# Kernel tuning notes

Measured on AMD Instinct MI355X. Metric: run time of the kernel, lower is better.

## Reference

```python
import itertools
import jax, jax.numpy as jnp
import numpy as np

# static block configuration
B, C, H, W, DIM, HEADS = 2, 4, 60, 120, 512, 8
WS = (2, 6, 12)          # window size (Wc, Wh, Ww)
SS = (1, 3, 6)           # shift size
N = WS[0] * WS[1] * WS[2]            # 144 tokens per window
C1, H1, W1 = C // WS[0], H // WS[1], W // WS[2]
NW = C1 * H1 * W1                    # windows per sample
DH = DIM // HEADS
EPS = 1e-6


def _attn_bias():
    """Static shifted-window attention bias (nW, N, N): 0 within group, -inf across.
    Mirrors compute_3d_shifted_window_mask (warped=True, longitude wrap merge)."""
    img = np.zeros((C, H, W), np.int32)
    c_sl = ((0, C - WS[0]), (C - WS[0], C - SS[0]), (C - SS[0], C))
    h_sl = ((0, H - WS[1]), (H - WS[1], H - SS[1]), (H - SS[1], H))
    w_sl = ((0, W - WS[2]), (W - WS[2], W - SS[2]), (W - SS[2], W))
    cnt = 0
    for (cs, ce), (hs, he), (ws_, we) in itertools.product(c_sl, h_sl, w_sl):
        img[cs:ce, hs:he, ws_:we] = cnt
        cnt += 1
    # warped (periodic longitude) group merges
    for i in range(3):
        for a, b in ((1, 2), (4, 5), (7, 8)):
            img[img == a + 9 * i] = b + 9 * i
    m = img.reshape(C1, WS[0], H1, WS[1], W1, WS[2])
    m = m.transpose(0, 2, 4, 1, 3, 5).reshape(NW, N)
    diff = m[:, None, :] - m[:, :, None]
    return jnp.asarray(np.where(diff != 0, -np.inf, 0.0).astype(np.float32))


_BIAS = _attn_bias()[None, :, None, :, :]  # (1, nW, 1, N, N)


def _ln(x, s, b):
    mu = x.mean(-1, keepdims=True)
    var = x.var(-1, keepdims=True)
    return (x - mu) / jnp.sqrt(var + EPS) * s + b


def setup_inputs() -> dict:
    key = jax.random.key(0)
    ks = jax.random.split(key, 6)
    s = 0.02
    return {
        "x": jax.random.normal(ks[0], (B, C * H * W, DIM), jnp.float32),
        "qkv_w": jax.random.normal(ks[1], (DIM, 3 * DIM), jnp.float32) * s,
        "qkv_b": jnp.zeros((3 * DIM,), jnp.float32),
        "proj_w": jax.random.normal(ks[2], (DIM, DIM), jnp.float32) * s,
        "proj_b": jnp.zeros((DIM,), jnp.float32),
        "norm1_scale": jnp.ones((DIM,), jnp.float32),
        "norm1_bias": jnp.zeros((DIM,), jnp.float32),
        "norm2_scale": jnp.ones((DIM,), jnp.float32),
        "norm2_bias": jnp.zeros((DIM,), jnp.float32),
        "mlp_w1": jax.random.normal(ks[3], (DIM, 4 * DIM), jnp.float32) * s,
        "mlp_b1": jnp.zeros((4 * DIM,), jnp.float32),
        "mlp_w2": jax.random.normal(ks[4], (4 * DIM, DIM), jnp.float32) * s,
        "mlp_b2": jnp.zeros((DIM,), jnp.float32),
    }


def reference(x, qkv_w, qkv_b, proj_w, proj_b, norm1_scale, norm1_bias,
              norm2_scale, norm2_bias, mlp_w1, mlp_b1, mlp_w2, mlp_b2):
    shortcut = x                                   # (B, L, D)
    h = _ln(x, norm1_scale, norm1_bias).reshape(B, C, H, W, DIM)
    # cyclic shift
    h = jnp.roll(h, (-SS[0], -SS[1], -SS[2]), axis=(1, 2, 3))
    # window partition: (B,C,H,W,D) -> (B*nW, N, D)
    h = h.reshape(B, C1, WS[0], H1, WS[1], W1, WS[2], DIM)
    h = h.transpose(0, 1, 3, 5, 2, 4, 6, 7).reshape(B * NW, N, DIM)
    # windowed multi-head self-attention
    qkv = h @ qkv_w + qkv_b                        # (B*nW, N, 3*D)
    qkv = qkv.reshape(B, NW, N, 3, HEADS, DH)
    q = qkv[..., 0, :, :].transpose(0, 1, 3, 2, 4)  # (B, nW, H, N, Dh)
    k = qkv[..., 1, :, :].transpose(0, 1, 3, 2, 4)
    v = qkv[..., 2, :, :].transpose(0, 1, 3, 2, 4)
    scale = 1.0 / float(np.sqrt(DH))
    attn = jnp.einsum("bwhnd,bwhmd->bwhnm", q, k) * scale + _BIAS
    attn = jax.nn.softmax(attn, axis=-1)
    o = jnp.einsum("bwhnm,bwhmd->bwhnd", attn, v)
    o = o.transpose(0, 1, 3, 2, 4).reshape(B * NW, N, DIM)
    o = o @ proj_w + proj_b
    # window reverse: (B*nW, N, D) -> (B,C,H,W,D)
    o = o.reshape(B, C1, H1, W1, WS[0], WS[1], WS[2], DIM)
    o = o.transpose(0, 1, 4, 2, 5, 3, 6, 7).reshape(B, C, H, W, DIM)
    # reverse cyclic shift
    o = jnp.roll(o, SS, axis=(1, 2, 3))
    x = shortcut + o.reshape(B, C * H * W, DIM)    # drop_path is identity
    # MLP block
    h2 = _ln(x, norm2_scale, norm2_bias)
    h2 = jax.nn.gelu(h2 @ mlp_w1 + mlp_b1) @ mlp_w2 + mlp_b2
    return x + h2
```

## Files before the change

kernel.cpp:

```cpp
#include <hip/hip_runtime.h>

typedef __attribute__((ext_vector_type(8))) short bf16x8;
typedef __attribute__((ext_vector_type(4))) float f32x4;
typedef __attribute__((ext_vector_type(8))) unsigned short u16x8;

#define BAR() __builtin_amdgcn_s_barrier()
#define VMC(n) asm volatile("s_waitcnt vmcnt(" #n ")" ::: "memory")
#define SB0() __builtin_amdgcn_sched_barrier(0)
#define WAITL() do { asm volatile("s_waitcnt lgkmcnt(0)"); SB0(); } while (0)
#define DSRI(dst, base, imm) \
  asm volatile("ds_read_b128 %0, %1 offset:%2" : "=&v"(dst) : "v"(base), "i"(imm))

__device__ inline unsigned short f2bf(float f) {
  unsigned int u = __float_as_uint(f);
  u += 0x7fffu + ((u >> 16) & 1u);
  return (unsigned short)(u >> 16);
}

__device__ inline void gload_lds16(const void* g, void* l) {
  __builtin_amdgcn_global_load_lds(
      (const __attribute__((address_space(1))) void*)g,
      (__attribute__((address_space(3))) void*)l, 16, 0, 0);
}

__global__ void wtrans(const float* __restrict__ W, unsigned short* __restrict__ Wt,
                       int K, int N) {
  int idx = blockIdx.x * 256 + threadIdx.x;
  if (idx >= K * N) return;
  int k = idx / N, n = idx - k * N;
  Wt[(size_t)n * K + k] = f2bf(W[idx]);
}

template <int MODE>
__global__ void ln_k(const float* __restrict__ x, const float* __restrict__ sc,
                     const float* __restrict__ bi, unsigned short* __restrict__ o) {
  int t = blockIdx.x * 4 + (threadIdx.x >> 6);
  int l = threadIdx.x & 63;
  size_t src;
  if (MODE == 0) {
    int b = t / 28800, r = t - b * 28800;
    int win = r / 144, tok = r - win * 144;
    int c1 = win / 100, rem = win - c1 * 100;
    int h1 = rem / 10, w1 = rem - h1 * 10;
    int tc = tok / 72, tr = tok - tc * 72;
    int th = tr / 12, tw = tr - th * 12;
    int cs = c1 * 2 + tc, hs = h1 * 6 + th, wsp = w1 * 12 + tw;
    int co = (cs + 1) & 3;
    int ho = hs + 3; if (ho >= 60) ho -= 60;
    int wo = wsp + 6; if (wo >= 120) wo -= 120;
    src = ((size_t)b * 28800 + (co * 60 + ho) * 120 + wo) * 512;
  } else {
    src = (size_t)t * 512;
  }
  const float4* xr = (const float4*)(x + src);
  float4 v0 = xr[l * 2], v1 = xr[l * 2 + 1];
  float s = v0.x + v0.y + v0.z + v0.w + v1.x + v1.y + v1.z + v1.w;
  float s2 = v0.x * v0.x + v0.y * v0.y + v0.z * v0.z + v0.w * v0.w +
             v1.x * v1.x + v1.y * v1.y + v1.z * v1.z + v1.w * v1.w;
  #pragma unroll
  for (int o2 = 32; o2; o2 >>= 1) {
    s += __shfl_xor(s, o2);
    s2 += __shfl_xor(s2, o2);
  }
  float mean = s * (1.0f / 512.0f);
  float var = s2 * (1.0f / 512.0f) - mean * mean;
  float inv = rsqrtf(var + 1e-6f);
  const float4* scp = (const float4*)sc;
  const float4* bip = (const float4*)bi;
  float4 sa = scp[l * 2], sb = scp[l * 2 + 1];
  float4 ba = bip[l * 2], bb = bip[l * 2 + 1];
  u16x8 ov;
  ov[0] = f2bf((v0.x - mean) * inv * sa.x + ba.x);
  ov[1] = f2bf((v0.y - mean) * inv * sa.y + ba.y);
  ov[2] = f2bf((v0.z - mean) * inv * sa.z + ba.z);
  ov[3] = f2bf((v0.w - mean) * inv * sa.w + ba.w);
  ov[4] = f2bf((v1.x - mean) * inv * sb.x + bb.x);
  ov[5] = f2bf((v1.y - mean) * inv * sb.y + bb.y);
  ov[6] = f2bf((v1.z - mean) * inv * sb.z + bb.z);
  ov[7] = f2bf((v1.w - mean) * inv * sb.w + bb.w);
  *(u16x8*)&o[(size_t)t * 512 + l * 8] = ov;
}

template <int EPI>
__launch_bounds__(256, 2)
__global__ void gemmB(const unsigned short* __restrict__ A,
                      const unsigned short* __restrict__ Bt,
                      const float* __restrict__ bias, void* __restrict__ outp,
                      const float* __restrict__ res, int M, int N, int K) {
  __shared__ __attribute__((aligned(16))) unsigned short ldsA[3][4096];
  const int tid = threadIdx.x;
  const int w = tid >> 6, l = tid & 63;
  const int lane15 = l & 15, lk = (l >> 4) << 3;
  const int ntile = N >> 8;
  const int nwg = gridDim.x;
  const int q = nwg >> 3, r = nwg & 7;
  const int xcd = blockIdx.x & 7, idx8 = blockIdx.x >> 3;
  const int wgid = (xcd < r ? xcd * (q + 1) : r * (q + 1) + (xcd - r) * q) + idx8;
  const int bm = wgid / ntile, bn = wgid - bm * ntile;
  const int KT = K >> 5;

  const int swzb = ((l >> 3) & 3) << 3;
  const int colx = (((l & 3) << 3) ^ swzb);
  const int offA0 = ((w * 16 + (l >> 2)) * K + colx) * 2;
  const int offA1 = (((4 + w) * 16 + (l >> 2)) * K + colx) * 2;

  const int sw = ((lane15 >> 1) & 3) << 3;
  unsigned lds0 = (unsigned)(unsigned long long)
      (__attribute__((address_space(3))) void*)(void*)&ldsA[0][0];
  unsigned bA0 = lds0 + (unsigned)(lane15 * 64 + ((lk ^ sw) << 1));
  unsigned bA1 = bA0 + 8192u, bA2 = bA0 + 16384u;
  unsigned short* p0 = &ldsA[0][0];
  unsigned short* p1 = &ldsA[1][0];
  unsigned short* p2 = &ldsA[2][0];

  const char* gA = (const char*)(A + (size_t)bm * 128 * K);

  const unsigned short* gBf[4];
  #pragma unroll
  for (int nf = 0; nf < 4; ++nf)
    gBf[nf] = Bt + (size_t)(bn * 256 + w * 64 + nf * 16 + lane15) * K + lk;

  f32x4 acc[8][4] = {};
  bf16x8 af[8], bP[4], bN[4];

  auto STAGEA = [&](unsigned short* pS, const char* ga) {
    gload_lds16(ga + offA0, pS + w * 512);
    gload_lds16(ga + offA1, pS + 2048 + w * 512);
  };
  auto MFMA32 = [&](bf16x8* bu) {
    __builtin_amdgcn_s_setprio(1);
    #pragma unroll
    for (int mi = 0; mi < 8; ++mi)
      #pragma unroll
      for (int nf = 0; nf < 4; ++nf)
        acc[mi][nf] = __builtin_amdgcn_mfma_f32_16x16x32_bf16(
            af[mi], bu[nf], acc[mi][nf], 0, 0, 0);
    __builtin_amdgcn_s_setprio(0);
  };

  STAGEA(p0, gA);
  STAGEA(p1, gA + 64);
  gA += 128;
  #pragma unroll
  for (int nf = 0; nf < 4; ++nf) { bP[nf] = *(const bf16x8*)gBf[nf]; gBf[nf] += 32; }
  VMC(0);
  BAR();

  for (int t = 0; t < KT; t += 2) {
    DSRI(af[0], bA0, 0);    DSRI(af[1], bA0, 1024);
    DSRI(af[2], bA0, 2048); DSRI(af[3], bA0, 3072);
    DSRI(af[4], bA0, 4096); DSRI(af[5], bA0, 5120);
    DSRI(af[6], bA0, 6144); DSRI(af[7], bA0, 7168);
    if (t + 2 < KT) { STAGEA(p2, gA); gA += 64; }
    if (t + 1 < KT) {
      #pragma unroll
      for (int nf = 0; nf < 4; ++nf) { bN[nf] = *(const bf16x8*)gBf[nf]; gBf[nf] += 32; }
    }
    if (t + 2 < KT) { VMC(6); } else if (t + 1 < KT) { VMC(4); } else { VMC(0); }
    WAITL();
    MFMA32(bP);
    BAR();
    { unsigned ta = bA0; bA0 = bA1; bA1 = bA2; bA2 = ta;
      unsigned short* tp = p0; p0 = p1; p1 = p2; p2 = tp; }
    DSRI(af[0], bA0, 0);    DSRI(af[1], bA0, 1024);
    DSRI(af[2], bA0, 2048); DSRI(af[3], bA0, 3072);
    DSRI(af[4], bA0, 4096); DSRI(af[5], bA0, 5120);
    DSRI(af[6], bA0, 6144); DSRI(af[7], bA0, 7168);
    if (t + 3 < KT) { STAGEA(p2, gA); gA += 64; }
    if (t + 2 < KT) {
      #pragma unroll
      for (int nf = 0; nf < 4; ++nf) { bP[nf] = *(const bf16x8*)gBf[nf]; gBf[nf] += 32; }
    }
    if (t + 3 < KT) { VMC(6); } else if (t + 2 < KT) { VMC(4); } else { VMC(0); }
    WAITL();
    MFMA32(bN);
    BAR();
    { unsigned ta = bA0; bA0 = bA1; bA1 = bA2; bA2 = ta;
      unsigned short* tp = p0; p0 = p1; p1 = p2; p2 = tp; }
  }

  float* outf = (float*)outp;
  unsigned short* outh = (unsigned short*)outp;
  #pragma unroll
  for (int mi = 0; mi < 8; ++mi) {
    #pragma unroll
    for (int j = 0; j < 4; ++j) {
      int grow = bm * 128 + mi * 16 + ((l >> 4) << 2) + j;
      int win = 0, tok = 0;
      size_t rowbase = 0;
      if constexpr (EPI == 0) {
        win = grow / 144;
        tok = grow - win * 144;
      } else if constexpr (EPI == 1) {
        win = grow / 144;
        tok = grow - win * 144;
        int b = win / 200, wl = win - b * 200;
        int c1 = wl / 100, rem = wl - c1 * 100;
        int h1 = rem / 10, w1 = rem - h1 * 10;
        int tc = tok / 72, tr = tok - tc * 72;
        int th = tr / 12, tw = tr - th * 12;
        int cs = c1 * 2 + tc, hs = h1 * 6 + th, wsp = w1 * 12 + tw;
        int co = (cs + 1) & 3;
        int ho = hs + 3; if (ho >= 60) ho -= 60;
        int wo = wsp + 6; if (wo >= 120) wo -= 120;
        rowbase = ((size_t)b * 28800 + (co * 60 + ho) * 120 + wo) * 512;
      }
      #pragma unroll
      for (int nf = 0; nf < 4; ++nf) {
        int gcol = bn * 256 + w * 64 + nf * 16 + lane15;
        float val = acc[mi][nf][j] + bias[gcol];
        if constexpr (EPI == 0) {
          int which = gcol >> 9, hd = (gcol >> 6) & 7, dh = gcol & 63;
          outh[(((size_t)(win * 3 + which) * 8 + hd) * 144 + tok) * 64 + dh] = f2bf(val);
        } else if constexpr (EPI == 1) {
          size_t oi = rowbase + gcol;
          outf[oi] = res[oi] + val;
        } else if constexpr (EPI == 2) {
          float u = 0.7978845608f * (val + 0.044715f * val * val * val);
          float g = val / (1.0f + __expf(-2.0f * u));
          outh[(size_t)grow * N + gcol] = f2bf(g);
        } else {
          size_t oi = (size_t)grow * N + gcol;
          outf[oi] += val;
        }
      }
    }
  }
}

__launch_bounds__(576)
__global__ void attn_k(const unsigned short* __restrict__ qkv,
                       unsigned short* __restrict__ owin) {
  __shared__ __attribute__((aligned(16))) unsigned short Ks[144 * 72];
  __shared__ __attribute__((aligned(16))) unsigned short Vt[64 * 168];
  __shared__ __attribute__((aligned(16))) unsigned short Ps[144 * 168];
  __shared__ unsigned char gid[144];
  int bid = blockIdx.x;
  int win = bid >> 3, head = bid & 7;
  const unsigned short* qb = qkv + ((size_t)(win * 3 + 0) * 8 + head) * (144 * 64);
  const unsigned short* kb = qkv + ((size_t)(win * 3 + 1) * 8 + head) * (144 * 64);
  const unsigned short* vb = qkv + ((size_t)(win * 3 + 2) * 8 + head) * (144 * 64);
  int tid = threadIdx.x;
  {
    int row = tid >> 2, c0 = (tid & 3) << 4;
    u16x8 ka = *(const u16x8*)(kb + row * 64 + c0);
    u16x8 kc = *(const u16x8*)(kb + row * 64 + c0 + 8);
    *(u16x8*)&Ks[row * 72 + c0] = ka;
    *(u16x8*)&Ks[row * 72 + c0 + 8] = kc;
    u16x8 va = *(const u16x8*)(vb + row * 64 + c0);
    u16x8 vc = *(const u16x8*)(vb + row * 64 + c0 + 8);
    #pragma unroll
    for (int j = 0; j < 8; ++j) Vt[(c0 + j) * 168 + row] = va[j];
    #pragma unroll
    for (int j = 0; j < 8; ++j) Vt[(c0 + 8 + j) * 168 + row] = vc[j];
  }
  for (int i = tid; i < 64 * 24; i += 576) {
    int d = i / 24, m = i - d * 24;
    Vt[d * 168 + 144 + m] = 0;
  }
  for (int i = tid; i < 144 * 24; i += 576) {
    int r = i / 24, c = i - r * 24;
    Ps[r * 168 + 144 + c] = 0;
  }
  if (tid < 144) {
    int wl = win % 200;
    int c1 = wl / 100, rem = wl - c1 * 100;
    int h1 = rem / 10, w1 = rem - h1 * 10;
    int tc = tid / 72, tr = tid - tc * 72;
    int th = tr / 12, tw = tr - th * 12;
    int cs = c1 * 2 + tc, hs = h1 * 6 + th, wsp = w1 * 12 + tw;
    int rc = cs < 2 ? 0 : (cs < 3 ? 1 : 2);
    int rh = hs < 54 ? 0 : (hs < 57 ? 1 : 2);
    int rw = wsp < 108 ? 0 : (wsp < 114 ? 1 : 2);
    if (rw == 1) rw = 2;
    gid[tid] = (unsigned char)(rc * 9 + rh * 3 + rw);
  }
  __syncthreads();
  int wv = tid >> 6, l = tid & 63;
  int lane15 = l & 15, lk = (l >> 4) << 3;
  bf16x8 aq0 = *(const bf16x8*)(qb + (wv * 16 + lane15) * 64 + lk);
  bf16x8 aq1 = *(const bf16x8*)(qb + (wv * 16 + lane15) * 64 + 32 + lk);
  f32x4 sf[9];
  #pragma unroll
  for (int ct = 0; ct < 9; ++ct) {
    f32x4 z = {};
    bf16x8 b0 = *(const bf16x8*)&Ks[(ct * 16 + lane15) * 72 + lk];
    bf16x8 b1 = *(const bf16x8*)&Ks[(ct * 16 + lane15) * 72 + 32 + lk];
    z = __builtin_amdgcn_mfma_f32_16x16x32_bf16(aq0, b0, z, 0, 0, 0);
    z = __builtin_amdgcn_mfma_f32_16x16x32_bf16(aq1, b1, z, 0, 0, 0);
    sf[ct] = z;
  }
  int gi[4];
  #pragma unroll
  for (int j = 0; j < 4; ++j) gi[j] = gid[wv * 16 + ((l >> 4) << 2) + j];
  float mx[4] = {-1e30f, -1e30f, -1e30f, -1e30f};
  #pragma unroll
  for (int ct = 0; ct < 9; ++ct) {
    int gj = gid[ct * 16 + lane15];
    #pragma unroll
    for (int j = 0; j < 4; ++j) {
      float s = sf[ct][j] * 0.125f;
      if (gj != gi[j]) s = -1e30f;
      sf[ct][j] = s;
      mx[j] = fmaxf(mx[j], s);
    }
  }
  #pragma unroll
  for (int o2 = 8; o2; o2 >>= 1)
    #pragma unroll
    for (int j = 0; j < 4; ++j) mx[j] = fmaxf(mx[j], __shfl_xor(mx[j], o2));
  float sm[4] = {0.f, 0.f, 0.f, 0.f};
  #pragma unroll
  for (int ct = 0; ct < 9; ++ct)
    #pragma unroll
    for (int j = 0; j < 4; ++j) {
      float e = __expf(sf[ct][j] - mx[j]);
      sf[ct][j] = e;
      sm[j] += e;
    }
  #pragma unroll
  for (int o2 = 8; o2; o2 >>= 1)
    #pragma unroll
    for (int j = 0; j < 4; ++j) sm[j] += __shfl_xor(sm[j], o2);
  float rs[4];
  #pragma unroll
  for (int j = 0; j < 4; ++j) rs[j] = 1.0f / sm[j];
  #pragma unroll
  for (int ct = 0; ct < 9; ++ct)
    #pragma unroll
    for (int j = 0; j < 4; ++j)
      Ps[(wv * 16 + ((l >> 4) << 2) + j) * 168 + ct * 16 + lane15] =
          f2bf(sf[ct][j] * rs[j]);
  __syncthreads();
  f32x4 of[4] = {};
  #pragma unroll
  for (int ks = 0; ks < 5; ++ks) {
    bf16x8 ap = *(const bf16x8*)&Ps[(wv * 16 + lane15) * 168 + ks * 32 + lk];
    #pragma unroll
    for (int nt = 0; nt < 4; ++nt) {
      bf16x8 bv = *(const bf16x8*)&Vt[(nt * 16 + lane15) * 168 + ks * 32 + lk];
      of[nt] = __builtin_amdgcn_mfma_f32_16x16x32_bf16(ap, bv, of[nt], 0, 0, 0);
    }
  }
  unsigned short* ob = owin + (size_t)win * 144 * 512 + head * 64;
  #pragma unroll
  for (int nt = 0; nt < 4; ++nt)
    #pragma unroll
    for (int j = 0; j < 4; ++j) {
      int row = wv * 16 + ((l >> 4) << 2) + j;
      ob[(size_t)row * 512 + nt * 16 + lane15] = f2bf(of[nt][j]);
    }
}

extern "C" void kernel_launch(void* const* d_in, const int* in_sizes, int n_in,
                              void* d_out, int out_size, void* d_ws, size_t ws_size,
                              hipStream_t stream) {
  const float* x = (const float*)d_in[0];
  const float* qkv_w = (const float*)d_in[1];
  const float* qkv_b = (const float*)d_in[2];
  const float* proj_w = (const float*)d_in[3];
  const float* proj_b = (const float*)d_in[4];
  const float* n1s = (const float*)d_in[5];
  const float* n1b = (const float*)d_in[6];
  const float* n2s = (const float*)d_in[7];
  const float* n2b = (const float*)d_in[8];
  const float* w1 = (const float*)d_in[9];
  const float* b1 = (const float*)d_in[10];
  const float* w2 = (const float*)d_in[11];
  const float* b2 = (const float*)d_in[12];
  float* out = (float*)d_out;
  char* ws = (char*)d_ws;

  unsigned short* WqT = (unsigned short*)(ws);
  unsigned short* WpT = (unsigned short*)(ws + 1572864);
  unsigned short* W1T = (unsigned short*)(ws + 2097152);
  unsigned short* W2T = (unsigned short*)(ws + 4194304);
  unsigned short* hwin = (unsigned short*)(ws + 6291456);
  unsigned short* qkvb = (unsigned short*)(ws + 65273856);
  unsigned short* owin = (unsigned short*)(ws + 242221056);
  unsigned short* mid = qkvb;

  wtrans<<<(512 * 1536 + 255) / 256, 256, 0, stream>>>(qkv_w, WqT, 512, 1536);
  wtrans<<<(512 * 512 + 255) / 256, 256, 0, stream>>>(proj_w, WpT, 512, 512);
  wtrans<<<(512 * 2048 + 255) / 256, 256, 0, stream>>>(w1, W1T, 512, 2048);
  wtrans<<<(2048 * 512 + 255) / 256, 256, 0, stream>>>(w2, W2T, 2048, 512);
  ln_k<0><<<14400, 256, 0, stream>>>(x, n1s, n1b, hwin);
  gemmB<0><<<450 * 6, 256, 0, stream>>>(hwin, WqT, qkv_b, qkvb, nullptr, 57600, 1536, 512);
  attn_k<<<3200, 576, 0, stream>>>(qkvb, owin);
  gemmB<1><<<450 * 2, 256, 0, stream>>>(owin, WpT, proj_b, out, x, 57600, 512, 512);
  ln_k<1><<<14400, 256, 0, stream>>>(out, n2s, n2b, hwin);
  gemmB<2><<<450 * 8, 256, 0, stream>>>(hwin, W1T, b1, mid, nullptr, 57600, 2048, 512);
  gemmB<3><<<450 * 2, 256, 0, stream>>>(mid, W2T, b2, out, nullptr, 57600, 512, 2048);
}
```

Before: 898.2 us.

## Rewrite GEMM as 256x256 tile with 8 waves and LDS-staged A and B

Replaces the 128x256 GEMM, which streams A through a triple-buffered LDS ring and loads B directly from global memory into registers, with a 256x256 tile run by 512 threads (8 waves in a 2x4 layout). Both A and B are now staged into a double-buffered, XOR-swizzled LDS buffer with K-step 64 via global_load_lds. The larger tile raises data reuse per block and removes the per-wave direct B loads. In exchange it uses 128KB of LDS per block, which with launch_bounds(512,2) risks low occupancy, and it issues a full vmcnt(0) wait plus a barrier on every K step.

```diff
diff --git a/kernel.cpp b/kernel.cpp
--- a/kernel.cpp
+++ b/kernel.cpp
@@ -7,7 +7,7 @@
 #define BAR() __builtin_amdgcn_s_barrier()
 #define VMC(n) asm volatile("s_waitcnt vmcnt(" #n ")" ::: "memory")
 #define SB0() __builtin_amdgcn_sched_barrier(0)
-#define WAITL() do { asm volatile("s_waitcnt lgkmcnt(0)"); SB0(); } while (0)
+#define WAITL(n) do { asm volatile("s_waitcnt lgkmcnt(" #n ")"); SB0(); } while (0)
 #define DSRI(dst, base, imm) \
   asm volatile("ds_read_b128 %0, %1 offset:%2" : "=&v"(dst) : "v"(base), "i"(imm))
 
@@ -82,101 +82,102 @@
 }
 
 template <int EPI>
-__launch_bounds__(256, 2)
-__global__ void gemmB(const unsigned short* __restrict__ A,
-                      const unsigned short* __restrict__ Bt,
-                      const float* __restrict__ bias, void* __restrict__ outp,
-                      const float* __restrict__ res, int M, int N, int K) {
-  __shared__ __attribute__((aligned(16))) unsigned short ldsA[3][4096];
+__launch_bounds__(512, 2)
+__global__ void gemm2p(const unsigned short* __restrict__ A,
+                       const unsigned short* __restrict__ Bt,
+                       const float* __restrict__ bias, void* __restrict__ outp,
+                       const float* __restrict__ res, int M, int N, int K) {
+  __shared__ __attribute__((aligned(16))) unsigned short ldsb[2][32768];
   const int tid = threadIdx.x;
   const int w = tid >> 6, l = tid & 63;
-  const int lane15 = l & 15, lk = (l >> 4) << 3;
+  const int wm = w >> 2, wn = w & 3;
+  const int lane15 = l & 15;
   const int ntile = N >> 8;
   const int nwg = gridDim.x;
   const int q = nwg >> 3, r = nwg & 7;
   const int xcd = blockIdx.x & 7, idx8 = blockIdx.x >> 3;
   const int wgid = (xcd < r ? xcd * (q + 1) : r * (q + 1) + (xcd - r) * q) + idx8;
   const int bm = wgid / ntile, bn = wgid - bm * ntile;
-  const int KT = K >> 5;
-
-  const int swzb = ((l >> 3) & 3) << 3;
-  const int colx = (((l & 3) << 3) ^ swzb);
-  const int offA0 = ((w * 16 + (l >> 2)) * K + colx) * 2;
-  const int offA1 = (((4 + w) * 16 + (l >> 2)) * K + colx) * 2;
-
-  const int sw = ((lane15 >> 1) & 3) << 3;
+  const int NT = K >> 6;
+
+  int offA[4];
+  {
+    int rowt = tid >> 3, slot = tid & 7;
+    int sl = slot ^ (rowt & 7);
+    #pragma unroll
+    for (int jj = 0; jj < 4; ++jj)
+      offA[jj] = ((jj * 64 + rowt) * K + sl * 8) * 2;
+  }
+  const char* gA = (const char*)(A + (size_t)bm * 256 * K);
+  const char* gB = (const char*)(Bt + (size_t)bn * 256 * K);
+
   unsigned lds0 = (unsigned)(unsigned long long)
-      (__attribute__((address_space(3))) void*)(void*)&ldsA[0][0];
-  unsigned bA0 = lds0 + (unsigned)(lane15 * 64 + ((lk ^ sw) << 1));
-  unsigned bA1 = bA0 + 8192u, bA2 = bA0 + 16384u;
-  unsigned short* p0 = &ldsA[0][0];
-  unsigned short* p1 = &ldsA[1][0];
-  unsigned short* p2 = &ldsA[2][0];
-
-  const char* gA = (const char*)(A + (size_t)bm * 128 * K);
-
-  const unsigned short* gBf[4];
-  #pragma unroll
-  for (int nf = 0; nf < 4; ++nf)
-    gBf[nf] = Bt + (size_t)(bn * 256 + w * 64 + nf * 16 + lane15) * K + lk;
+      (__attribute__((address_space(3))) void*)(void*)&ldsb[0][0];
+  const int rsw = (((l >> 4) ^ (lane15 & 7)) << 4);
+  unsigned rA0 = lds0 + (unsigned)((wm * 128 + lane15) * 128 + rsw);
+  unsigned rB0 = lds0 + 32768u + (unsigned)((wn * 64 + lane15) * 128 + rsw);
+  unsigned rA1 = rA0 + 65536u, rB1 = rB0 + 65536u;
+  unsigned short* pC = &ldsb[0][0];
+  unsigned short* pN = &ldsb[1][0];
 
   f32x4 acc[8][4] = {};
-  bf16x8 af[8], bP[4], bN[4];
-
-  auto STAGEA = [&](unsigned short* pS, const char* ga) {
-    gload_lds16(ga + offA0, pS + w * 512);
-    gload_lds16(ga + offA1, pS + 2048 + w * 512);
+  bf16x8 af[8], bf[4], ag[8], bg[4];
+
+  auto STAGE = [&](unsigned short* pS) {
+    #pragma unroll
+    for (int jj = 0; jj < 4; ++jj)
+      gload_lds16(gA + offA[jj], pS + jj * 4096 + tid * 8);
+    #pragma unroll
+    for (int jj = 0; jj < 4; ++jj)
+      gload_lds16(gB + offA[jj], pS + 16384 + jj * 4096 + tid * 8);
+    gA += 128;
+    gB += 128;
   };
-  auto MFMA32 = [&](bf16x8* bu) {
+
+  STAGE(pC);
+  VMC(0);
+  BAR();
+
+  for (int t = 0; t < NT; ++t) {
+    if (t < NT - 1) STAGE(pN);
+    DSRI(af[0], rA0, 0);    DSRI(af[1], rA0, 2048);
+    DSRI(af[2], rA0, 4096); DSRI(af[3], rA0, 6144);
+    DSRI(af[4], rA0, 8192); DSRI(af[5], rA0, 10240);
+    DSRI(af[6], rA0, 12288); DSRI(af[7], rA0, 14336);
+    DSRI(bf[0], rB0, 0);    DSRI(bf[1], rB0, 2048);
+    DSRI(bf[2], rB0, 4096); DSRI(bf[3], rB0, 6144);
+    {
+      unsigned rAx = rA0 ^ 64u, rBx = rB0 ^ 64u;
+      DSRI(ag[0], rAx, 0);    DSRI(ag[1], rAx, 2048);
+      DSRI(ag[2], rAx, 4096); DSRI(ag[3], rAx, 6144);
+      DSRI(ag[4], rAx, 8192); DSRI(ag[5], rAx, 10240);
+      DSRI(ag[6], rAx, 12288); DSRI(ag[7], rAx, 14336);
+      DSRI(bg[0], rBx, 0);    DSRI(bg[1], rBx, 2048);
+      DSRI(bg[2], rBx, 4096); DSRI(bg[3], rBx, 6144);
+    }
+    WAITL(12);
     __builtin_amdgcn_s_setprio(1);
     #pragma unroll
     for (int mi = 0; mi < 8; ++mi)
       #pragma unroll
       for (int nf = 0; nf < 4; ++nf)
         acc[mi][nf] = __builtin_amdgcn_mfma_f32_16x16x32_bf16(
-            af[mi], bu[nf], acc[mi][nf], 0, 0, 0);
+            af[mi], bf[nf], acc[mi][nf], 0, 0, 0);
     __builtin_amdgcn_s_setprio(0);
-  };
-
-  STAGEA(p0, gA);
-  STAGEA(p1, gA + 64);
-  gA += 128;
-  #pragma unroll
-  for (int nf = 0; nf < 4; ++nf) { bP[nf] = *(const bf16x8*)gBf[nf]; gBf[nf] += 32; }
-  VMC(0);
-  BAR();
-
-  for (int t = 0; t < KT; t += 2) {
-    DSRI(af[0], bA0, 0);    DSRI(af[1], bA0, 1024);
-    DSRI(af[2], bA0, 2048); DSRI(af[3], bA0, 3072);
-    DSRI(af[4], bA0, 4096); DSRI(af[5], bA0, 5120);
-    DSRI(af[6], bA0, 6144); DSRI(af[7], bA0, 7168);
-    if (t + 2 < KT) { STAGEA(p2, gA); gA += 64; }
-    if (t + 1 < KT) {
+    WAITL(0);
+    __builtin_amdgcn_s_setprio(1);
+    #pragma unroll
+    for (int mi = 0; mi < 8; ++mi)
       #pragma unroll
-      for (int nf = 0; nf < 4; ++nf) { bN[nf] = *(const bf16x8*)gBf[nf]; gBf[nf] += 32; }
-    }
-    if (t + 2 < KT) { VMC(6); } else if (t + 1 < KT) { VMC(4); } else { VMC(0); }
-    WAITL();
-    MFMA32(bP);
+      for (int nf = 0; nf < 4; ++nf)
+        acc[mi][nf] = __builtin_amdgcn_mfma_f32_16x16x32_bf16(
+            ag[mi], bg[nf], acc[mi][nf], 0, 0, 0);
+    __builtin_amdgcn_s_setprio(0);
+    VMC(0);
     BAR();
-    { unsigned ta = bA0; bA0 = bA1; bA1 = bA2; bA2 = ta;
-      unsigned short* tp = p0; p0 = p1; p1 = p2; p2 = tp; }
-    DSRI(af[0], bA0, 0);    DSRI(af[1], bA0, 1024);
-    DSRI(af[2], bA0, 2048); DSRI(af[3], bA0, 3072);
-    DSRI(af[4], bA0, 4096); DSRI(af[5], bA0, 5120);
-    DSRI(af[6], bA0, 6144); DSRI(af[7], bA0, 7168);
-    if (t + 3 < KT) { STAGEA(p2, gA); gA += 64; }
-    if (t + 2 < KT) {
-      #pragma unroll
-      for (int nf = 0; nf < 4; ++nf) { bP[nf] = *(const bf16x8*)gBf[nf]; gBf[nf] += 32; }
-    }
-    if (t + 3 < KT) { VMC(6); } else if (t + 2 < KT) { VMC(4); } else { VMC(0); }
-    WAITL();
-    MFMA32(bN);
-    BAR();
-    { unsigned ta = bA0; bA0 = bA1; bA1 = bA2; bA2 = ta;
-      unsigned short* tp = p0; p0 = p1; p1 = p2; p2 = tp; }
+    { unsigned tt = rA0; rA0 = rA1; rA1 = tt; }
+    { unsigned tt = rB0; rB0 = rB1; rB1 = tt; }
+    { unsigned short* tp = pC; pC = pN; pN = tp; }
   }
 
   float* outf = (float*)outp;
@@ -185,7 +186,7 @@
   for (int mi = 0; mi < 8; ++mi) {
     #pragma unroll
     for (int j = 0; j < 4; ++j) {
-      int grow = bm * 128 + mi * 16 + ((l >> 4) << 2) + j;
+      int grow = bm * 256 + wm * 128 + mi * 16 + ((l >> 4) << 2) + j;
       int win = 0, tok = 0;
       size_t rowbase = 0;
       if constexpr (EPI == 0) {
@@ -207,7 +208,7 @@
       }
       #pragma unroll
       for (int nf = 0; nf < 4; ++nf) {
-        int gcol = bn * 256 + w * 64 + nf * 16 + lane15;
+        int gcol = bn * 256 + wn * 64 + nf * 16 + lane15;
         float val = acc[mi][nf][j] + bias[gcol];
         if constexpr (EPI == 0) {
           int which = gcol >> 9, hd = (gcol >> 6) & 7, dh = gcol & 63;
@@ -385,10 +386,10 @@
   wtrans<<<(512 * 2048 + 255) / 256, 256, 0, stream>>>(w1, W1T, 512, 2048);
   wtrans<<<(2048 * 512 + 255) / 256, 256, 0, stream>>>(w2, W2T, 2048, 512);
   ln_k<0><<<14400, 256, 0, stream>>>(x, n1s, n1b, hwin);
-  gemmB<0><<<450 * 6, 256, 0, stream>>>(hwin, WqT, qkv_b, qkvb, nullptr, 57600, 1536, 512);
+  gemm2p<0><<<225 * 6, 512, 0, stream>>>(hwin, WqT, qkv_b, qkvb, nullptr, 57600, 1536, 512);
   attn_k<<<3200, 576, 0, stream>>>(qkvb, owin);
-  gemmB<1><<<450 * 2, 256, 0, stream>>>(owin, WpT, proj_b, out, x, 57600, 512, 512);
+  gemm2p<1><<<225 * 2, 512, 0, stream>>>(owin, WpT, proj_b, out, x, 57600, 512, 512);
   ln_k<1><<<14400, 256, 0, stream>>>(out, n2s, n2b, hwin);
-  gemmB<2><<<450 * 8, 256, 0, stream>>>(hwin, W1T, b1, mid, nullptr, 57600, 2048, 512);
-  gemmB<3><<<450 * 2, 256, 0, stream>>>(mid, W2T, b2, out, nullptr, 57600, 512, 2048);
-}
+  gemm2p<2><<<225 * 8, 512, 0, stream>>>(hwin, W1T, b1, mid, nullptr, 57600, 2048, 512);
+  gemm2p<3><<<225 * 2, 512, 0, stream>>>(mid, W2T, b2, out, nullptr, 57600, 512, 2048);
+}
```

Result: faster. 790.7 us (-12.0%).

## Interleave LDS A-fragment reads with MFMAs and deepen B register prefetch

Applied to the files above, without the earlier changes.

Restructures the GEMM main loop so the eight A-fragment LDS reads are interleaved with the MFMA groups through two rotating registers and lgkmcnt(1) waits, replacing the previous pattern of issuing all reads and then waiting. B fragments now rotate through four register buffers, prefetched two k-steps ahead, and the loop is unrolled by four. The aim is to hide LDS and global latency behind matrix math and to cut register pressure from holding eight A fragments. This relies on KT being a multiple of four, and the vmcnt accounting becomes more delicate.

```diff
diff --git a/kernel.cpp b/kernel.cpp
--- a/kernel.cpp
+++ b/kernel.cpp
@@ -7,9 +7,16 @@
 #define BAR() __builtin_amdgcn_s_barrier()
 #define VMC(n) asm volatile("s_waitcnt vmcnt(" #n ")" ::: "memory")
 #define SB0() __builtin_amdgcn_sched_barrier(0)
-#define WAITL() do { asm volatile("s_waitcnt lgkmcnt(0)"); SB0(); } while (0)
+#define L1() do { asm volatile("s_waitcnt lgkmcnt(1)"); SB0(); } while (0)
+#define L0() do { asm volatile("s_waitcnt lgkmcnt(0)"); SB0(); } while (0)
 #define DSRI(dst, base, imm) \
   asm volatile("ds_read_b128 %0, %1 offset:%2" : "=&v"(dst) : "v"(base), "i"(imm))
+#define MFMA4(i, x, bb) do { \
+  acc[i][0] = __builtin_amdgcn_mfma_f32_16x16x32_bf16(x, bb[0], acc[i][0], 0, 0, 0); \
+  acc[i][1] = __builtin_amdgcn_mfma_f32_16x16x32_bf16(x, bb[1], acc[i][1], 0, 0, 0); \
+  acc[i][2] = __builtin_amdgcn_mfma_f32_16x16x32_bf16(x, bb[2], acc[i][2], 0, 0, 0); \
+  acc[i][3] = __builtin_amdgcn_mfma_f32_16x16x32_bf16(x, bb[3], acc[i][3], 0, 0, 0); \
+} while (0)
 
 __device__ inline unsigned short f2bf(float f) {
   unsigned int u = __float_as_uint(f);
@@ -83,7 +90,7 @@
 
 template <int EPI>
 __launch_bounds__(256, 2)
-__global__ void gemmB(const unsigned short* __restrict__ A,
+__global__ void gemmD(const unsigned short* __restrict__ A,
                       const unsigned short* __restrict__ Bt,
                       const float* __restrict__ bias, void* __restrict__ outp,
                       const float* __restrict__ res, int M, int N, int K) {
@@ -112,71 +119,56 @@
   unsigned short* p0 = &ldsA[0][0];
   unsigned short* p1 = &ldsA[1][0];
   unsigned short* p2 = &ldsA[2][0];
-
   const char* gA = (const char*)(A + (size_t)bm * 128 * K);
 
-  const unsigned short* gBf[4];
+  const unsigned short* pB[4];
   #pragma unroll
   for (int nf = 0; nf < 4; ++nf)
-    gBf[nf] = Bt + (size_t)(bn * 256 + w * 64 + nf * 16 + lane15) * K + lk;
+    pB[nf] = Bt + (size_t)(bn * 256 + w * 64 + nf * 16 + lane15) * K + lk;
 
   f32x4 acc[8][4] = {};
-  bf16x8 af[8], bP[4], bN[4];
+  bf16x8 b0[4], b1[4], b2[4], b3[4];
 
   auto STAGEA = [&](unsigned short* pS, const char* ga) {
     gload_lds16(ga + offA0, pS + w * 512);
     gload_lds16(ga + offA1, pS + 2048 + w * 512);
   };
-  auto MFMA32 = [&](bf16x8* bu) {
+  auto LOADB = [&](bf16x8 (&bl)[4]) {
+    #pragma unroll
+    for (int nf = 0; nf < 4; ++nf) { bl[nf] = *(const bf16x8*)pB[nf]; pB[nf] += 32; }
+  };
+
+  STAGEA(p0, gA); LOADB(b0);
+  STAGEA(p1, gA + 64); LOADB(b1);
+  VMC(6);
+  BAR();
+
+  auto BODY = [&](int t, bf16x8 (&bu)[4], bf16x8 (&bl)[4]) {
+    const bool st = (t + 2 < KT);
+    if (st) { LOADB(bl); STAGEA(p2, gA + (size_t)(t + 2) * 64); }
+    bf16x8 u, v;
+    DSRI(u, bA0, 0); DSRI(v, bA0, 1024);
     __builtin_amdgcn_s_setprio(1);
-    #pragma unroll
-    for (int mi = 0; mi < 8; ++mi)
-      #pragma unroll
-      for (int nf = 0; nf < 4; ++nf)
-        acc[mi][nf] = __builtin_amdgcn_mfma_f32_16x16x32_bf16(
-            af[mi], bu[nf], acc[mi][nf], 0, 0, 0);
+    L1(); MFMA4(0, u, bu); DSRI(u, bA0, 2048);
+    L1(); MFMA4(1, v, bu); DSRI(v, bA0, 3072);
+    L1(); MFMA4(2, u, bu); DSRI(u, bA0, 4096);
+    L1(); MFMA4(3, v, bu); DSRI(v, bA0, 5120);
+    L1(); MFMA4(4, u, bu); DSRI(u, bA0, 6144);
+    L1(); MFMA4(5, v, bu); DSRI(v, bA0, 7168);
+    L1(); MFMA4(6, u, bu);
+    L0(); MFMA4(7, v, bu);
     __builtin_amdgcn_s_setprio(0);
+    if (st) { VMC(6); } else if (t + 1 < KT) { VMC(0); }
+    BAR();
+    unsigned ta = bA0; bA0 = bA1; bA1 = bA2; bA2 = ta;
+    unsigned short* tp = p0; p0 = p1; p1 = p2; p2 = tp;
   };
 
-  STAGEA(p0, gA);
-  STAGEA(p1, gA + 64);
-  gA += 128;
-  #pragma unroll
-  for (int nf = 0; nf < 4; ++nf) { bP[nf] = *(const bf16x8*)gBf[nf]; gBf[nf] += 32; }
-  VMC(0);
-  BAR();
-
-  for (int t = 0; t < KT; t += 2) {
-    DSRI(af[0], bA0, 0);    DSRI(af[1], bA0, 1024);
-    DSRI(af[2], bA0, 2048); DSRI(af[3], bA0, 3072);
-    DSRI(af[4], bA0, 4096); DSRI(af[5], bA0, 5120);
-    DSRI(af[6], bA0, 6144); DSRI(af[7], bA0, 7168);
-    if (t + 2 < KT) { STAGEA(p2, gA); gA += 64; }
-    if (t + 1 < KT) {
-      #pragma unroll
-      for (int nf = 0; nf < 4; ++nf) { bN[nf] = *(const bf16x8*)gBf[nf]; gBf[nf] += 32; }
-    }
-    if (t + 2 < KT) { VMC(6); } else if (t + 1 < KT) { VMC(4); } else { VMC(0); }
-    WAITL();
-    MFMA32(bP);
-    BAR();
-    { unsigned ta = bA0; bA0 = bA1; bA1 = bA2; bA2 = ta;
-      unsigned short* tp = p0; p0 = p1; p1 = p2; p2 = tp; }
-    DSRI(af[0], bA0, 0);    DSRI(af[1], bA0, 1024);
-    DSRI(af[2], bA0, 2048); DSRI(af[3], bA0, 3072);
-    DSRI(af[4], bA0, 4096); DSRI(af[5], bA0, 5120);
-    DSRI(af[6], bA0, 6144); DSRI(af[7], bA0, 7168);
-    if (t + 3 < KT) { STAGEA(p2, gA); gA += 64; }
-    if (t + 2 < KT) {
-      #pragma unroll
-      for (int nf = 0; nf < 4; ++nf) { bP[nf] = *(const bf16x8*)gBf[nf]; gBf[nf] += 32; }
-    }
-    if (t + 3 < KT) { VMC(6); } else if (t + 2 < KT) { VMC(4); } else { VMC(0); }
-    WAITL();
-    MFMA32(bN);
-    BAR();
-    { unsigned ta = bA0; bA0 = bA1; bA1 = bA2; bA2 = ta;
-      unsigned short* tp = p0; p0 = p1; p1 = p2; p2 = tp; }
+  for (int t4 = 0; t4 < KT; t4 += 4) {
+    BODY(t4 + 0, b0, b2);
+    BODY(t4 + 1, b1, b3);
+    BODY(t4 + 2, b2, b0);
+    BODY(t4 + 3, b3, b1);
   }
 
   float* outf = (float*)outp;
@@ -385,10 +377,10 @@
   wtrans<<<(512 * 2048 + 255) / 256, 256, 0, stream>>>(w1, W1T, 512, 2048);
   wtrans<<<(2048 * 512 + 255) / 256, 256, 0, stream>>>(w2, W2T, 2048, 512);
   ln_k<0><<<14400, 256, 0, stream>>>(x, n1s, n1b, hwin);
-  gemmB<0><<<450 * 6, 256, 0, stream>>>(hwin, WqT, qkv_b, qkvb, nullptr, 57600, 1536, 512);
+  gemmD<0><<<450 * 6, 256, 0, stream>>>(hwin, WqT, qkv_b, qkvb, nullptr, 57600, 1536, 512);
   attn_k<<<3200, 576, 0, stream>>>(qkvb, owin);
-  gemmB<1><<<450 * 2, 256, 0, stream>>>(owin, WpT, proj_b, out, x, 57600, 512, 512);
+  gemmD<1><<<450 * 2, 256, 0, stream>>>(owin, WpT, proj_b, out, x, 57600, 512, 512);
   ln_k<1><<<14400, 256, 0, stream>>>(out, n2s, n2b, hwin);
-  gemmB<2><<<450 * 8, 256, 0, stream>>>(hwin, W1T, b1, mid, nullptr, 57600, 2048, 512);
-  gemmB<3><<<450 * 2, 256, 0, stream>>>(mid, W2T, b2, out, nullptr, 57600, 512, 2048);
-}
+  gemmD<2><<<450 * 8, 256, 0, stream>>>(hwin, W1T, b1, mid, nullptr, 57600, 2048, 512);
+  gemmD<3><<<450 * 2, 256, 0, stream>>>(mid, W2T, b2, out, nullptr, 57600, 512, 2048);
+}
```

New measurement: 1.413 ms. 1.57x slower.
